# Optimization experiments

Hardware: AMD Instinct MI355X
Metric: run time of the kernel (lower is better)

The kernel has to match this reference:

```python
import jax, jax.numpy as jnp
import numpy as np
from jax import lax


def setup_inputs() -> dict:
    key = jax.random.key(0)
    ks = jax.random.split(key, 8)
    B, N, q = 16, 4096, 256
    sc = float(1.0 / np.sqrt(q))
    return {
        "u": jax.random.normal(ks[0], (B, N, q), jnp.float32),
        "a": jax.random.normal(ks[1], (q,), jnp.float32),  # diag of A
        "W_B": jax.random.normal(ks[2], (q, q), jnp.float32) * sc,
        "b_B": jax.random.normal(ks[3], (q,), jnp.float32) * sc,
        "W_C": jax.random.normal(ks[4], (q, q), jnp.float32) * sc,
        "b_C": jax.random.normal(ks[5], (q,), jnp.float32) * sc,
        "W_D": jax.random.normal(ks[6], (q, q), jnp.float32) * sc,
        "b_D": jax.random.normal(ks[7], (q,), jnp.float32) * sc,
    }


def _solve_im(u, a, W_B, b_B, dt):
    """IM solver. A is diagonal, so M_inv is four diagonal blocks:
    new_x = s*x - dt*s*a*z ; new_z = dt*s*x + s*z, with s = 1/(1+dt^2*a).
    Forcing F = M_inv @ [dt*B(u); 0] -> (dt*s*Bu, dt^2*s*Bu)."""
    s = 1.0 / (1.0 + dt * dt * a)  # (q,)
    Bu = jnp.einsum("bnq,pq->bnp", u, W_B) + b_B  # (B,N,q), torch Linear: u @ W^T + b
    f_x = (dt * s) * Bu
    f_z = (dt * dt * s) * Bu
    dsa = dt * s * a
    ds = dt * s

    def step(carry, f):
        x, z = carry
        fx, fz = f
        x_new = s * x - dsa * z + fx
        z_new = ds * x + s * z + fz
        return (x_new, z_new), z_new

    Bsz, _, q = u.shape
    init = (jnp.zeros((Bsz, q), u.dtype), jnp.zeros((Bsz, q), u.dtype))
    # scan over time axis
    _, z_t = lax.scan(step, init, (jnp.moveaxis(f_x, 1, 0), jnp.moveaxis(f_z, 1, 0)))
    return jnp.moveaxis(z_t, 0, 1)  # (B,N,q) -- the out[..., size:] half


def reference(u, a, W_B, b_B, W_C, b_C, W_D, b_D):
    N = u.shape[1]
    dt = 1.0 / N
    y = _solve_im(u, a, W_B, b_B, dt)
    x = (jnp.einsum("bnq,pq->bnp", y, W_C) + b_C) + (jnp.einsum("bnq,pq->bnp", u, W_D) + b_D)
    x = jax.nn.gelu(x, approximate=False)  # torch GELU default = exact erf
    # GLU(concat([x, x], -1)) == x * sigmoid(x)
    out = x * jax.nn.sigmoid(x) + u
    return (out, y)
```

## Files before the change

### kernel.cpp

```cpp
#include <hip/hip_runtime.h>
#include <hip/hip_bf16.h>
#include <cstdint>

typedef __bf16 bf16_t;
typedef __bf16 bf16x8 __attribute__((ext_vector_type(8)));
typedef float f32x4 __attribute__((ext_vector_type(4)));

#define B_SZ 16
#define N_SZ 4096
#define Q_SZ 256
#define M_TOT (B_SZ * N_SZ)
#define DT (1.0f / 4096.0f)
#define LDST 40
#define CHUNKS 64
#define LOG2_CLEN 6
#define CLEN (N_SZ / CHUNKS)
#define PF 8


__device__ __forceinline__ bf16x8 load8f(const float* p) {
  const float4 v0 = *(const float4*)p;
  const float4 v1 = *(const float4*)(p + 4);
  bf16x8 v;
  v[0] = (bf16_t)v0.x; v[1] = (bf16_t)v0.y; v[2] = (bf16_t)v0.z; v[3] = (bf16_t)v0.w;
  v[4] = (bf16_t)v1.x; v[5] = (bf16_t)v1.y; v[6] = (bf16_t)v1.z; v[7] = (bf16_t)v1.w;
  return v;
}

__device__ __forceinline__ int pidx(int tm, int tk, int lane) {
  return ((tm * 8 + tk) * 64 + lane) * 8;
}


__device__ __forceinline__ void kpassP(const bf16_t* __restrict__ A,
                                       const bf16_t* __restrict__ Bw,
                                       int tmA, int tnB, int lane,
                                       f32x4 acc[4][4]) {
#pragma unroll
  for (int tk = 0; tk < 8; ++tk) {
    bf16x8 af[4], bv[4];
#pragma unroll
    for (int i = 0; i < 4; ++i) {
      af[i] = *(const bf16x8*)(A + pidx(tmA + i, tk, lane));
      bv[i] = *(const bf16x8*)(Bw + pidx(tnB + i, tk, lane));
    }
#pragma unroll
    for (int mi = 0; mi < 4; ++mi)
#pragma unroll
      for (int ni = 0; ni < 4; ++ni)
        acc[mi][ni] = __builtin_amdgcn_mfma_f32_16x16x32_bf16(af[mi], bv[ni],
                                                              acc[mi][ni], 0, 0, 0);
  }
}

__device__ __forceinline__ void kpass2P(const bf16_t* __restrict__ A1,
                                        const bf16_t* __restrict__ B1,
                                        const bf16_t* __restrict__ A2,
                                        const bf16_t* __restrict__ B2,
                                        int tmA, int tnB, int lane,
                                        f32x4 acc[4][4]) {
#pragma unroll
  for (int tk = 0; tk < 8; ++tk) {
    bf16x8 a1[4], b1[4], a2[4], b2[4];
#pragma unroll
    for (int i = 0; i < 4; ++i) {
      a1[i] = *(const bf16x8*)(A1 + pidx(tmA + i, tk, lane));
      b1[i] = *(const bf16x8*)(B1 + pidx(tnB + i, tk, lane));
      a2[i] = *(const bf16x8*)(A2 + pidx(tmA + i, tk, lane));
      b2[i] = *(const bf16x8*)(B2 + pidx(tnB + i, tk, lane));
    }
#pragma unroll
    for (int mi = 0; mi < 4; ++mi)
#pragma unroll
      for (int ni = 0; ni < 4; ++ni)
        acc[mi][ni] = __builtin_amdgcn_mfma_f32_16x16x32_bf16(a1[mi], b1[ni],
                                                              acc[mi][ni], 0, 0, 0);
#pragma unroll
    for (int mi = 0; mi < 4; ++mi)
#pragma unroll
      for (int ni = 0; ni < 4; ++ni)
        acc[mi][ni] = __builtin_amdgcn_mfma_f32_16x16x32_bf16(a2[mi], b2[ni],
                                                              acc[mi][ni], 0, 0, 0);
  }
}

__global__ __launch_bounds__(256) void prep_kernel(
    const float* __restrict__ u, const float* __restrict__ WB,
    const float* __restrict__ WC, const float* __restrict__ WD,
    bf16_t* __restrict__ ubP, bf16_t* __restrict__ WBbP,
    bf16_t* __restrict__ WCbP, bf16_t* __restrict__ WDbP) {
  const int g = blockIdx.x * 256 + threadIdx.x;
  const int UC = (M_TOT * Q_SZ) / 8;
  const float* src;
  bf16_t* dst;
  int cidx;
  if (g < UC) {
    src = u; dst = ubP; cidx = g;
  } else {
    const int h = g - UC;
    const int w = h >> 13;
    cidx = h & 8191;
    src = (w == 0) ? WB : (w == 1) ? WC : WD;
    dst = (w == 0) ? WBbP : (w == 1) ? WCbP : WDbP;
  }
  const int lane = cidx & 63, tk = (cidx >> 6) & 7, tm = cidx >> 9;
  const int row = tm * 16 + (lane & 15);
  const int col = tk * 32 + (lane >> 4) * 8;
  *(bf16x8*)(dst + (size_t)cidx * 8) = load8f(src + (size_t)row * Q_SZ + col);
}

__global__ __launch_bounds__(256, 2) void gemm1p_kernel(
    const bf16_t* __restrict__ ubP, const bf16_t* __restrict__ WBbP,
    const float* __restrict__ a, const float* __restrict__ bB,
    float* __restrict__ fx) {
  const int t = threadIdx.x;
  const int bid = blockIdx.x;
  const int swz = (bid & 7) * 128 + (bid >> 3);
  const int m0 = (swz >> 1) * 128, n0 = (swz & 1) * 128;
  const int lane = t & 63, ln = lane & 15, quad = lane >> 4;
  const int wave = t >> 6;
  const int wm = (wave & 1) * 64, wn = (wave >> 1) * 64;
  f32x4 acc[4][4] = {};
  kpassP(ubP, WBbP, (m0 + wm) >> 4, (n0 + wn) >> 4, lane, acc);
#pragma unroll
  for (int ni = 0; ni < 4; ++ni) {
    const int gp = n0 + wn + ni * 16 + ln;
    const float av = a[gp];
    const float s = 1.0f / (1.0f + DT * DT * av);
    const float sc = DT * s;
    const float bb = bB[gp];
#pragma unroll
    for (int mi = 0; mi < 4; ++mi) {
      const int gm = m0 + wm + mi * 16 + quad * 4;
#pragma unroll
      for (int r2 = 0; r2 < 4; ++r2)
        fx[(size_t)(gm + r2) * Q_SZ + gp] = sc * (acc[mi][ni][r2] + bb);
    }
  }
}

__global__ __launch_bounds__(256, 2) void gemm2p_kernel(
    const bf16_t* __restrict__ ybP, const bf16_t* __restrict__ WCbP,
    const bf16_t* __restrict__ ubP, const bf16_t* __restrict__ WDbP,
    const float* __restrict__ u, const float* __restrict__ bC,
    const float* __restrict__ bD, float* __restrict__ out0) {
  const int t = threadIdx.x;
  const int bid = blockIdx.x;
  const int swz = (bid & 7) * 128 + (bid >> 3);
  const int m0 = (swz >> 1) * 128, n0 = (swz & 1) * 128;
  const int lane = t & 63, ln = lane & 15, quad = lane >> 4;
  const int wave = t >> 6;
  const int wm = (wave & 1) * 64, wn = (wave >> 1) * 64;
  f32x4 acc[4][4] = {};
  kpass2P(ybP, WCbP, ubP, WDbP, (m0 + wm) >> 4, (n0 + wn) >> 4, lane, acc);
#pragma unroll
  for (int ni = 0; ni < 4; ++ni) {
    const int gp = n0 + wn + ni * 16 + ln;
    const float bias = bC[gp] + bD[gp];
#pragma unroll
    for (int mi = 0; mi < 4; ++mi) {
      const int gm = m0 + wm + mi * 16 + quad * 4;
#pragma unroll
      for (int r2 = 0; r2 < 4; ++r2) {
        const float x = acc[mi][ni][r2] + bias;
        const float g = 0.5f * x * (1.0f + erff(x * 0.70710678118654752f));
        const float sg = 1.0f / (1.0f + __expf(-g));
        const float uu = u[(size_t)(gm + r2) * Q_SZ + gp];
        out0[(size_t)(gm + r2) * Q_SZ + gp] = fmaf(g, sg, uu);
      }
    }
  }
}


__global__ __launch_bounds__(256) void scan1_kernel(
    const float* __restrict__ fx, const float* __restrict__ a,
    float* __restrict__ ex, float* __restrict__ ez) {
  const int g = blockIdx.x * 256 + threadIdx.x;
  const int p = g & 255, c = (g >> 8) & (CHUNKS - 1), b = g >> 14;
  const float av = a[p];
  const float s = 1.0f / (1.0f + DT * DT * av);
  const float dsa = DT * s * av, dss = DT * s;
  float x = 0.f, z = 0.f;
  const float* fp = fx + ((size_t)b * N_SZ + c * CLEN) * Q_SZ + p;
  float buf[PF], nbuf[PF];
#pragma unroll
  for (int j = 0; j < PF; ++j) buf[j] = fp[(size_t)j * Q_SZ];
  for (int n = 0; n < CLEN; n += PF) {
    if (n + PF < CLEN) {
#pragma unroll
      for (int j = 0; j < PF; ++j) nbuf[j] = fp[(size_t)(n + PF + j) * Q_SZ];
    }
#pragma unroll
    for (int j = 0; j < PF; ++j) {
      const float f = buf[j];
      const float xn = fmaf(s, x, fmaf(-dsa, z, f));
      const float zn = fmaf(dss, x, fmaf(s, z, DT * f));
      x = xn; z = zn;
    }
#pragma unroll
    for (int j = 0; j < PF; ++j) buf[j] = nbuf[j];
  }
  ex[g] = x; ez[g] = z;
}

__global__ __launch_bounds__(256) void scan2_kernel(
    const float* __restrict__ a, const float* __restrict__ ex,
    const float* __restrict__ ez, float* __restrict__ ix, float* __restrict__ iz) {
  const int g = blockIdx.x * 256 + threadIdx.x;
  const int p = g & 255, b = g >> 8;
  const float av = a[p];
  const float s = 1.0f / (1.0f + DT * DT * av);
  float m00 = s, m01 = -DT * s * av, m10 = DT * s, m11 = s;
#pragma unroll
  for (int i = 0; i < LOG2_CLEN; ++i) {
    const float a00 = fmaf(m00, m00, m01 * m10);
    const float a01 = m01 * (m00 + m11);
    const float a10 = m10 * (m00 + m11);
    const float a11 = fmaf(m11, m11, m01 * m10);
    m00 = a00; m01 = a01; m10 = a10; m11 = a11;
  }
  float x = 0.f, z = 0.f;
  for (int c = 0; c < CHUNKS; ++c) {
    const size_t idx = ((size_t)b * CHUNKS + c) * Q_SZ + p;
    ix[idx] = x; iz[idx] = z;
    const float xn = fmaf(m00, x, fmaf(m01, z, ex[idx]));
    const float zn = fmaf(m10, x, fmaf(m11, z, ez[idx]));
    x = xn; z = zn;
  }
}

__global__ __launch_bounds__(256) void scan3_kernel(
    const float* __restrict__ a, const float* __restrict__ ix,
    const float* __restrict__ iz, float* __restrict__ yf,
    bf16_t* __restrict__ yb) {
  const int g = blockIdx.x * 256 + threadIdx.x;
  const int p = g & 255, c = (g >> 8) & (CHUNKS - 1), b = g >> 14;
  const float av = a[p];
  const float s = 1.0f / (1.0f + DT * DT * av);
  const float dsa = DT * s * av, dss = DT * s;
  float x = ix[g], z = iz[g];
  const size_t base = ((size_t)b * N_SZ + c * CLEN) * Q_SZ + p;
  float* yp = yf + base;
  const int tk = p >> 5, quad = (p >> 3) & 3, off = p & 7;
  const size_t ybase =
      ((size_t)(b * 256 + c * 4)) * 4096 + tk * 512 + quad * 128 + off;
  float buf[PF], nbuf[PF];
#pragma unroll
  for (int j = 0; j < PF; ++j) buf[j] = yp[(size_t)j * Q_SZ];
  for (int n = 0; n < CLEN; n += PF) {
    if (n + PF < CLEN) {
#pragma unroll
      for (int j = 0; j < PF; ++j) nbuf[j] = yp[(size_t)(n + PF + j) * Q_SZ];
    }
#pragma unroll
    for (int j = 0; j < PF; ++j) {
      const float f = buf[j];
      const float xn = fmaf(s, x, fmaf(-dsa, z, f));
      const float zn = fmaf(dss, x, fmaf(s, z, DT * f));
      x = xn; z = zn;
      yp[(size_t)(n + j) * Q_SZ] = zn;
      if (yb) {
        const int nj = n + j;
        yb[ybase + ((size_t)(nj >> 4) << 12) + ((nj & 15) << 3)] = (bf16_t)zn;
      }
    }
#pragma unroll
    for (int j = 0; j < PF; ++j) buf[j] = nbuf[j];
  }
}

__global__ __launch_bounds__(256) void scan_mono_kernel(
    const float* __restrict__ a, float* __restrict__ yf) {
  const int g = blockIdx.x * 256 + threadIdx.x;
  const int p = g & 255, b = g >> 8;
  const float av = a[p];
  const float s = 1.0f / (1.0f + DT * DT * av);
  const float dsa = DT * s * av, dss = DT * s;
  float x = 0.f, z = 0.f;
  float* yp = yf + (size_t)b * N_SZ * Q_SZ + p;
  float buf[PF], nbuf[PF];
#pragma unroll
  for (int j = 0; j < PF; ++j) buf[j] = yp[(size_t)j * Q_SZ];
  for (int n = 0; n < N_SZ; n += PF) {
    if (n + PF < N_SZ) {
#pragma unroll
      for (int j = 0; j < PF; ++j) nbuf[j] = yp[(size_t)(n + PF + j) * Q_SZ];
    }
#pragma unroll
    for (int j = 0; j < PF; ++j) {
      const float f = buf[j];
      const float xn = fmaf(s, x, fmaf(-dsa, z, f));
      const float zn = fmaf(dss, x, fmaf(s, z, DT * f));
      x = xn; z = zn;
      yp[(size_t)(n + j) * Q_SZ] = zn;
    }
#pragma unroll
    for (int j = 0; j < PF; ++j) buf[j] = nbuf[j];
  }
}


__device__ __forceinline__ void kloop(const float* __restrict__ Ap,
                                      const float* __restrict__ Bp,
                                      int m0, int n0, int t,
                                      bf16_t* As, bf16_t* Bs, f32x4 acc[4][4]) {
  const int r = t >> 2, cc = t & 3;
  const int lane = t & 63, ln = lane & 15, quad = lane >> 4;
  const int wave = t >> 6;
  const int wm = (wave & 1) * 64, wn = (wave >> 1) * 64;

  for (int k0 = 0; k0 < Q_SZ; k0 += 32) {
#pragma unroll
    for (int i = 0; i < 2; ++i) {
      const int row = r + i * 64;
      const int col = k0 + cc * 8;
      *(bf16x8*)(As + row * LDST + cc * 8) =
          load8f(Ap + (size_t)(m0 + row) * Q_SZ + col);
      *(bf16x8*)(Bs + row * LDST + cc * 8) =
          load8f(Bp + (size_t)(n0 + row) * Q_SZ + col);
    }
    __syncthreads();
    bf16x8 af[4], bv[4];
#pragma unroll
    for (int mi = 0; mi < 4; ++mi) {
      af[mi] = *(const bf16x8*)(As + (wm + mi * 16 + ln) * LDST + quad * 8);
      bv[mi] = *(const bf16x8*)(Bs + (wn + mi * 16 + ln) * LDST + quad * 8);
    }
#pragma unroll
    for (int mi = 0; mi < 4; ++mi)
#pragma unroll
      for (int ni = 0; ni < 4; ++ni)
        acc[mi][ni] = __builtin_amdgcn_mfma_f32_16x16x32_bf16(af[mi], bv[ni],
                                                              acc[mi][ni], 0, 0, 0);
    __syncthreads();
  }
}

__global__ __launch_bounds__(256) void gemm1_kernel(
    const float* __restrict__ u, const float* __restrict__ WB,
    const float* __restrict__ a, const float* __restrict__ bB,
    float* __restrict__ fx) {
  __shared__ __align__(16) bf16_t As[128 * LDST];
  __shared__ __align__(16) bf16_t Bs[128 * LDST];
  const int t = threadIdx.x;
  const int m0 = blockIdx.x * 128, n0 = blockIdx.y * 128;
  f32x4 acc[4][4] = {};
  kloop(u, WB, m0, n0, t, As, Bs, acc);

  const int lane = t & 63, ln = lane & 15, quad = lane >> 4;
  const int wave = t >> 6;
  const int wm = (wave & 1) * 64, wn = (wave >> 1) * 64;
#pragma unroll
  for (int ni = 0; ni < 4; ++ni) {
    const int gp = n0 + wn + ni * 16 + ln;
    const float av = a[gp];
    const float s = 1.0f / (1.0f + DT * DT * av);
    const float sc = DT * s;
    const float bb = bB[gp];
#pragma unroll
    for (int mi = 0; mi < 4; ++mi) {
      const int gm = m0 + wm + mi * 16 + quad * 4;
#pragma unroll
      for (int r2 = 0; r2 < 4; ++r2)
        fx[(size_t)(gm + r2) * Q_SZ + gp] = sc * (acc[mi][ni][r2] + bb);
    }
  }
}

__global__ __launch_bounds__(256) void gemm2_kernel(
    const float* __restrict__ y, const float* __restrict__ WC,
    const float* __restrict__ u, const float* __restrict__ WD,
    const float* __restrict__ bC, const float* __restrict__ bD,
    float* __restrict__ out0) {
  __shared__ __align__(16) bf16_t As[128 * LDST];
  __shared__ __align__(16) bf16_t Bs[128 * LDST];
  const int t = threadIdx.x;
  const int m0 = blockIdx.x * 128, n0 = blockIdx.y * 128;
  f32x4 acc[4][4] = {};
  kloop(y, WC, m0, n0, t, As, Bs, acc);
  kloop(u, WD, m0, n0, t, As, Bs, acc);

  const int lane = t & 63, ln = lane & 15, quad = lane >> 4;
  const int wave = t >> 6;
  const int wm = (wave & 1) * 64, wn = (wave >> 1) * 64;
#pragma unroll
  for (int ni = 0; ni < 4; ++ni) {
    const int gp = n0 + wn + ni * 16 + ln;
    const float bias = bC[gp] + bD[gp];
#pragma unroll
    for (int mi = 0; mi < 4; ++mi) {
      const int gm = m0 + wm + mi * 16 + quad * 4;
#pragma unroll
      for (int r2 = 0; r2 < 4; ++r2) {
        const float x = acc[mi][ni][r2] + bias;
        const float g = 0.5f * x * (1.0f + erff(x * 0.70710678118654752f));
        const float sg = 1.0f / (1.0f + __expf(-g));
        const float uu = u[(size_t)(gm + r2) * Q_SZ + gp];
        out0[(size_t)(gm + r2) * Q_SZ + gp] = fmaf(g, sg, uu);
      }
    }
  }
}


extern "C" void kernel_launch(void* const* d_in, const int* in_sizes, int n_in,
                              void* d_out, int out_size, void* d_ws, size_t ws_size,
                              hipStream_t stream) {
  const float* u  = (const float*)d_in[0];
  const float* a  = (const float*)d_in[1];
  const float* WB = (const float*)d_in[2];
  const float* bB = (const float*)d_in[3];
  const float* WC = (const float*)d_in[4];
  const float* bC = (const float*)d_in[5];
  const float* WD = (const float*)d_in[6];
  const float* bD = (const float*)d_in[7];

  float* out0 = (float*)d_out;
  float* yreg = out0 + (size_t)M_TOT * Q_SZ;

  const size_t UB_ELEMS = (size_t)M_TOT * Q_SZ;
  const size_t W_ELEMS = (size_t)Q_SZ * Q_SZ;
  const size_t state_bytes =
      4 * (size_t)B_SZ * CHUNKS * Q_SZ * sizeof(float);
  const size_t need_full =
      (2 * UB_ELEMS + 3 * W_ELEMS) * sizeof(bf16_t) + state_bytes;

  if (ws_size >= need_full) {
    bf16_t* ubP  = (bf16_t*)d_ws;
    bf16_t* ybP  = ubP + UB_ELEMS;
    bf16_t* WBbP = ybP + UB_ELEMS;
    bf16_t* WCbP = WBbP + W_ELEMS;
    bf16_t* WDbP = WCbP + W_ELEMS;
    float* ex = (float*)(WDbP + W_ELEMS);
    float* ez = ex + (size_t)B_SZ * CHUNKS * Q_SZ;
    float* ix = ez + (size_t)B_SZ * CHUNKS * Q_SZ;
    float* iz = ix + (size_t)B_SZ * CHUNKS * Q_SZ;

    prep_kernel<<<8288, 256, 0, stream>>>(u, WB, WC, WD, ubP, WBbP, WCbP, WDbP);
    gemm1p_kernel<<<1024, 256, 0, stream>>>(ubP, WBbP, a, bB, yreg);
    scan1_kernel<<<1024, 256, 0, stream>>>(yreg, a, ex, ez);
    scan2_kernel<<<16, 256, 0, stream>>>(a, ex, ez, ix, iz);
    scan3_kernel<<<1024, 256, 0, stream>>>(a, ix, iz, yreg, ybP);
    gemm2p_kernel<<<1024, 256, 0, stream>>>(ybP, WCbP, ubP, WDbP, u, bC, bD, out0);
  } else {
    dim3 gg(M_TOT / 128, Q_SZ / 128);
    gemm1_kernel<<<gg, 256, 0, stream>>>(u, WB, a, bB, yreg);
    if (ws_size >= state_bytes) {
      float* ex = (float*)d_ws;
      float* ez = ex + (size_t)B_SZ * CHUNKS * Q_SZ;
      float* ix = ez + (size_t)B_SZ * CHUNKS * Q_SZ;
      float* iz = ix + (size_t)B_SZ * CHUNKS * Q_SZ;
      scan1_kernel<<<1024, 256, 0, stream>>>(yreg, a, ex, ez);
      scan2_kernel<<<16, 256, 0, stream>>>(a, ex, ez, ix, iz);
      scan3_kernel<<<1024, 256, 0, stream>>>(a, ix, iz, yreg, (bf16_t*)nullptr);
    } else {
      scan_mono_kernel<<<16, 256, 0, stream>>>(a, yreg);
    }
    gemm2_kernel<<<gg, 256, 0, stream>>>(yreg, WC, u, WD, bC, bD, out0);
  }
}
```

Before: 331.0 us.

## Fuse chunk scan into GEMM epilogues using precomputed transition-matrix powers

The first GEMM now runs the local 64-step chunk scan in its epilogue through shared memory. It writes zero-initial local z values in a packed fp32 layout plus the chunk end states, so the separate scan1 kernel and the full fx round trip go away. A tiny kernel computes powers of the 2x2 transition matrix, and the second GEMM fixes up each local z with the carried-in chunk state (y = lz + T10*ix + T11*iz) while loading its A operand. It also converts to bf16 on the fly and writes y, removing scan3 and the bf16 y buffer. The cost is an fp32 lz buffer read inside the GEMM, extra loads for the correction terms, and a 64-step serial scan inside a GEMM block.

```diff
diff --git a/kernel.cpp b/kernel.cpp
--- a/kernel.cpp
+++ b/kernel.cpp
@@ -31,7 +31,6 @@
   return ((tm * 8 + tk) * 64 + lane) * 8;
 }
 
-
 __device__ __forceinline__ void kpassP(const bf16_t* __restrict__ A,
                                        const bf16_t* __restrict__ Bw,
                                        int tmA, int tnB, int lane,
@@ -49,37 +48,6 @@
 #pragma unroll
       for (int ni = 0; ni < 4; ++ni)
         acc[mi][ni] = __builtin_amdgcn_mfma_f32_16x16x32_bf16(af[mi], bv[ni],
-                                                              acc[mi][ni], 0, 0, 0);
-  }
-}
-
-__device__ __forceinline__ void kpass2P(const bf16_t* __restrict__ A1,
-                                        const bf16_t* __restrict__ B1,
-                                        const bf16_t* __restrict__ A2,
-                                        const bf16_t* __restrict__ B2,
-                                        int tmA, int tnB, int lane,
-                                        f32x4 acc[4][4]) {
-#pragma unroll
-  for (int tk = 0; tk < 8; ++tk) {
-    bf16x8 a1[4], b1[4], a2[4], b2[4];
-#pragma unroll
-    for (int i = 0; i < 4; ++i) {
-      a1[i] = *(const bf16x8*)(A1 + pidx(tmA + i, tk, lane));
-      b1[i] = *(const bf16x8*)(B1 + pidx(tnB + i, tk, lane));
-      a2[i] = *(const bf16x8*)(A2 + pidx(tmA + i, tk, lane));
-      b2[i] = *(const bf16x8*)(B2 + pidx(tnB + i, tk, lane));
-    }
-#pragma unroll
-    for (int mi = 0; mi < 4; ++mi)
-#pragma unroll
-      for (int ni = 0; ni < 4; ++ni)
-        acc[mi][ni] = __builtin_amdgcn_mfma_f32_16x16x32_bf16(a1[mi], b1[ni],
-                                                              acc[mi][ni], 0, 0, 0);
-#pragma unroll
-    for (int mi = 0; mi < 4; ++mi)
-#pragma unroll
-      for (int ni = 0; ni < 4; ++ni)
-        acc[mi][ni] = __builtin_amdgcn_mfma_f32_16x16x32_bf16(a2[mi], b2[ni],
                                                               acc[mi][ni], 0, 0, 0);
   }
 }
@@ -109,10 +77,12 @@
   *(bf16x8*)(dst + (size_t)cidx * 8) = load8f(src + (size_t)row * Q_SZ + col);
 }
 
-__global__ __launch_bounds__(256, 2) void gemm1p_kernel(
+__global__ __launch_bounds__(256, 2) void gemm1f_kernel(
     const bf16_t* __restrict__ ubP, const bf16_t* __restrict__ WBbP,
     const float* __restrict__ a, const float* __restrict__ bB,
-    float* __restrict__ fx) {
+    float* __restrict__ ex, float* __restrict__ ez,
+    float* __restrict__ lzP) {
+  __shared__ float T[2][64][128];
   const int t = threadIdx.x;
   const int bid = blockIdx.x;
   const int swz = (bid & 7) * 128 + (bid >> 3);
@@ -122,86 +92,50 @@
   const int wm = (wave & 1) * 64, wn = (wave >> 1) * 64;
   f32x4 acc[4][4] = {};
   kpassP(ubP, WBbP, (m0 + wm) >> 4, (n0 + wn) >> 4, lane, acc);
+
+  const int cc = wave & 1;
 #pragma unroll
   for (int ni = 0; ni < 4; ++ni) {
-    const int gp = n0 + wn + ni * 16 + ln;
+    const int colL = wn + ni * 16 + ln;
+    const int gp = n0 + colL;
     const float av = a[gp];
     const float s = 1.0f / (1.0f + DT * DT * av);
     const float sc = DT * s;
     const float bb = bB[gp];
 #pragma unroll
     for (int mi = 0; mi < 4; ++mi) {
-      const int gm = m0 + wm + mi * 16 + quad * 4;
+      const int nrow = mi * 16 + quad * 4;
 #pragma unroll
       for (int r2 = 0; r2 < 4; ++r2)
-        fx[(size_t)(gm + r2) * Q_SZ + gp] = sc * (acc[mi][ni][r2] + bb);
-    }
-  }
-}
-
-__global__ __launch_bounds__(256, 2) void gemm2p_kernel(
-    const bf16_t* __restrict__ ybP, const bf16_t* __restrict__ WCbP,
-    const bf16_t* __restrict__ ubP, const bf16_t* __restrict__ WDbP,
-    const float* __restrict__ u, const float* __restrict__ bC,
-    const float* __restrict__ bD, float* __restrict__ out0) {
-  const int t = threadIdx.x;
-  const int bid = blockIdx.x;
-  const int swz = (bid & 7) * 128 + (bid >> 3);
-  const int m0 = (swz >> 1) * 128, n0 = (swz & 1) * 128;
-  const int lane = t & 63, ln = lane & 15, quad = lane >> 4;
-  const int wave = t >> 6;
-  const int wm = (wave & 1) * 64, wn = (wave >> 1) * 64;
-  f32x4 acc[4][4] = {};
-  kpass2P(ybP, WCbP, ubP, WDbP, (m0 + wm) >> 4, (n0 + wn) >> 4, lane, acc);
-#pragma unroll
-  for (int ni = 0; ni < 4; ++ni) {
-    const int gp = n0 + wn + ni * 16 + ln;
-    const float bias = bC[gp] + bD[gp];
-#pragma unroll
-    for (int mi = 0; mi < 4; ++mi) {
-      const int gm = m0 + wm + mi * 16 + quad * 4;
-#pragma unroll
-      for (int r2 = 0; r2 < 4; ++r2) {
-        const float x = acc[mi][ni][r2] + bias;
-        const float g = 0.5f * x * (1.0f + erff(x * 0.70710678118654752f));
-        const float sg = 1.0f / (1.0f + __expf(-g));
-        const float uu = u[(size_t)(gm + r2) * Q_SZ + gp];
-        out0[(size_t)(gm + r2) * Q_SZ + gp] = fmaf(g, sg, uu);
-      }
-    }
-  }
-}
-
-
-__global__ __launch_bounds__(256) void scan1_kernel(
-    const float* __restrict__ fx, const float* __restrict__ a,
-    float* __restrict__ ex, float* __restrict__ ez) {
-  const int g = blockIdx.x * 256 + threadIdx.x;
-  const int p = g & 255, c = (g >> 8) & (CHUNKS - 1), b = g >> 14;
-  const float av = a[p];
-  const float s = 1.0f / (1.0f + DT * DT * av);
-  const float dsa = DT * s * av, dss = DT * s;
-  float x = 0.f, z = 0.f;
-  const float* fp = fx + ((size_t)b * N_SZ + c * CLEN) * Q_SZ + p;
-  float buf[PF], nbuf[PF];
-#pragma unroll
-  for (int j = 0; j < PF; ++j) buf[j] = fp[(size_t)j * Q_SZ];
-  for (int n = 0; n < CLEN; n += PF) {
-    if (n + PF < CLEN) {
-#pragma unroll
-      for (int j = 0; j < PF; ++j) nbuf[j] = fp[(size_t)(n + PF + j) * Q_SZ];
-    }
-#pragma unroll
-    for (int j = 0; j < PF; ++j) {
-      const float f = buf[j];
+        T[cc][nrow + r2][colL] = sc * (acc[mi][ni][r2] + bb);
+    }
+  }
+  __syncthreads();
+
+  const int scc = t >> 7, col = t & 127;
+  const int pg = n0 + col;
+  {
+    const float av = a[pg];
+    const float s = 1.0f / (1.0f + DT * DT * av);
+    const float dsa = DT * s * av, dss = DT * s;
+    const int mbase = m0 + scc * 64;
+    const int tkp = pg >> 5, e = pg & 7;
+    const int plane = (((pg >> 3) & 3) << 4);
+    float x = 0.f, z = 0.f;
+#pragma unroll 8
+    for (int n = 0; n < 64; ++n) {
+      const float f = T[scc][n][col];
       const float xn = fmaf(s, x, fmaf(-dsa, z, f));
       const float zn = fmaf(dss, x, fmaf(s, z, DT * f));
       x = xn; z = zn;
-    }
-#pragma unroll
-    for (int j = 0; j < PF; ++j) buf[j] = nbuf[j];
-  }
-  ex[g] = x; ez[g] = z;
+      const int m = mbase + n;
+      const int tm = m >> 4;
+      lzP[(size_t)(((tm * 8 + tkp) * 64 + (plane | (m & 15)))) * 8 + e] = zn;
+    }
+    const int chunk_g = mbase >> 6;
+    ex[chunk_g * 256 + pg] = x;
+    ez[chunk_g * 256 + pg] = z;
+  }
 }
 
 __global__ __launch_bounds__(256) void scan2_kernel(
@@ -230,73 +164,112 @@
   }
 }
 
-__global__ __launch_bounds__(256) void scan3_kernel(
-    const float* __restrict__ a, const float* __restrict__ ix,
-    const float* __restrict__ iz, float* __restrict__ yf,
-    bf16_t* __restrict__ yb) {
-  const int g = blockIdx.x * 256 + threadIdx.x;
-  const int p = g & 255, c = (g >> 8) & (CHUNKS - 1), b = g >> 14;
+__global__ __launch_bounds__(256) void mpow_kernel(
+    const float* __restrict__ a, float* __restrict__ t10,
+    float* __restrict__ t11) {
+  const int p = threadIdx.x;
   const float av = a[p];
   const float s = 1.0f / (1.0f + DT * DT * av);
-  const float dsa = DT * s * av, dss = DT * s;
-  float x = ix[g], z = iz[g];
-  const size_t base = ((size_t)b * N_SZ + c * CLEN) * Q_SZ + p;
-  float* yp = yf + base;
-  const int tk = p >> 5, quad = (p >> 3) & 3, off = p & 7;
-  const size_t ybase =
-      ((size_t)(b * 256 + c * 4)) * 4096 + tk * 512 + quad * 128 + off;
-  float buf[PF], nbuf[PF];
-#pragma unroll
-  for (int j = 0; j < PF; ++j) buf[j] = yp[(size_t)j * Q_SZ];
-  for (int n = 0; n < CLEN; n += PF) {
-    if (n + PF < CLEN) {
-#pragma unroll
-      for (int j = 0; j < PF; ++j) nbuf[j] = yp[(size_t)(n + PF + j) * Q_SZ];
-    }
-#pragma unroll
-    for (int j = 0; j < PF; ++j) {
-      const float f = buf[j];
-      const float xn = fmaf(s, x, fmaf(-dsa, z, f));
-      const float zn = fmaf(dss, x, fmaf(s, z, DT * f));
-      x = xn; z = zn;
-      yp[(size_t)(n + j) * Q_SZ] = zn;
-      if (yb) {
-        const int nj = n + j;
-        yb[ybase + ((size_t)(nj >> 4) << 12) + ((nj & 15) << 3)] = (bf16_t)zn;
+  const float m00 = s, m01 = -DT * s * av, m10 = DT * s, m11 = s;
+  float p00 = m00, p01 = m01, p10 = m10, p11 = m11;
+  for (int n = 0; n < 64; ++n) {
+    t10[n * 256 + p] = p10;
+    t11[n * 256 + p] = p11;
+    const float q00 = fmaf(m00, p00, m01 * p10);
+    const float q01 = fmaf(m00, p01, m01 * p11);
+    const float q10 = fmaf(m10, p00, m11 * p10);
+    const float q11 = fmaf(m10, p01, m11 * p11);
+    p00 = q00; p01 = q01; p10 = q10; p11 = q11;
+  }
+}
+
+__global__ __launch_bounds__(256, 2) void gemm2f_kernel(
+    const float* __restrict__ lzP, const bf16_t* __restrict__ WCbP,
+    const bf16_t* __restrict__ ubP, const bf16_t* __restrict__ WDbP,
+    const float* __restrict__ ix, const float* __restrict__ iz,
+    const float* __restrict__ t10, const float* __restrict__ t11,
+    const float* __restrict__ u, const float* __restrict__ bC,
+    const float* __restrict__ bD, float* __restrict__ yout,
+    float* __restrict__ out0) {
+  const int t = threadIdx.x;
+  const int bid = blockIdx.x;
+  const int swz = (bid & 7) * 128 + (bid >> 3);
+  const int m0 = (swz >> 1) * 128, n0 = (swz & 1) * 128;
+  const int lane = t & 63, ln = lane & 15, quad = lane >> 4;
+  const int wave = t >> 6;
+  const int wm = (wave & 1) * 64, wn = (wave >> 1) * 64;
+  const int tmA = (m0 + wm) >> 4, tnB = (n0 + wn) >> 4;
+  const bool wY = (n0 == 0) && (wn == 0);
+  f32x4 acc[4][4] = {};
+#pragma unroll
+  for (int tk = 0; tk < 8; ++tk) {
+    bf16x8 af[4], bv[4], a2[4], b2[4];
+#pragma unroll
+    for (int i = 0; i < 4; ++i) {
+      const float* lp = lzP + (size_t)(((tmA + i) * 8 + tk) * 64 + lane) * 8;
+      const f32x4 l0 = *(const f32x4*)lp;
+      const f32x4 l1 = *(const f32x4*)(lp + 4);
+      const int m = (tmA + i) * 16 + ln;
+      const int nloc = m & 63, cg = m >> 6;
+      const int p0 = tk * 32 + quad * 8;
+      const f32x4 tA0 = *(const f32x4*)(t10 + nloc * 256 + p0);
+      const f32x4 tA1 = *(const f32x4*)(t10 + nloc * 256 + p0 + 4);
+      const f32x4 tB0 = *(const f32x4*)(t11 + nloc * 256 + p0);
+      const f32x4 tB1 = *(const f32x4*)(t11 + nloc * 256 + p0 + 4);
+      const f32x4 X0 = *(const f32x4*)(ix + cg * 256 + p0);
+      const f32x4 X1 = *(const f32x4*)(ix + cg * 256 + p0 + 4);
+      const f32x4 Z0 = *(const f32x4*)(iz + cg * 256 + p0);
+      const f32x4 Z1 = *(const f32x4*)(iz + cg * 256 + p0 + 4);
+      f32x4 y0, y1;
+#pragma unroll
+      for (int e = 0; e < 4; ++e) {
+        y0[e] = fmaf(tA0[e], X0[e], fmaf(tB0[e], Z0[e], l0[e]));
+        y1[e] = fmaf(tA1[e], X1[e], fmaf(tB1[e], Z1[e], l1[e]));
       }
-    }
-#pragma unroll
-    for (int j = 0; j < PF; ++j) buf[j] = nbuf[j];
-  }
-}
-
-__global__ __launch_bounds__(256) void scan_mono_kernel(
-    const float* __restrict__ a, float* __restrict__ yf) {
-  const int g = blockIdx.x * 256 + threadIdx.x;
-  const int p = g & 255, b = g >> 8;
-  const float av = a[p];
-  const float s = 1.0f / (1.0f + DT * DT * av);
-  const float dsa = DT * s * av, dss = DT * s;
-  float x = 0.f, z = 0.f;
-  float* yp = yf + (size_t)b * N_SZ * Q_SZ + p;
-  float buf[PF], nbuf[PF];
-#pragma unroll
-  for (int j = 0; j < PF; ++j) buf[j] = yp[(size_t)j * Q_SZ];
-  for (int n = 0; n < N_SZ; n += PF) {
-    if (n + PF < N_SZ) {
-#pragma unroll
-      for (int j = 0; j < PF; ++j) nbuf[j] = yp[(size_t)(n + PF + j) * Q_SZ];
-    }
-#pragma unroll
-    for (int j = 0; j < PF; ++j) {
-      const float f = buf[j];
-      const float xn = fmaf(s, x, fmaf(-dsa, z, f));
-      const float zn = fmaf(dss, x, fmaf(s, z, DT * f));
-      x = xn; z = zn;
-      yp[(size_t)(n + j) * Q_SZ] = zn;
-    }
-#pragma unroll
-    for (int j = 0; j < PF; ++j) buf[j] = nbuf[j];
+      if (wY) {
+        *(f32x4*)(yout + (size_t)m * Q_SZ + p0) = y0;
+        *(f32x4*)(yout + (size_t)m * Q_SZ + p0 + 4) = y1;
+      }
+      bf16x8 av_;
+#pragma unroll
+      for (int e = 0; e < 4; ++e) {
+        av_[e] = (bf16_t)y0[e];
+        av_[e + 4] = (bf16_t)y1[e];
+      }
+      af[i] = av_;
+      a2[i] = *(const bf16x8*)(ubP + pidx(tmA + i, tk, lane));
+      bv[i] = *(const bf16x8*)(WCbP + pidx(tnB + i, tk, lane));
+      b2[i] = *(const bf16x8*)(WDbP + pidx(tnB + i, tk, lane));
+    }
+#pragma unroll
+    for (int mi = 0; mi < 4; ++mi)
+#pragma unroll
+      for (int ni = 0; ni < 4; ++ni)
+        acc[mi][ni] = __builtin_amdgcn_mfma_f32_16x16x32_bf16(af[mi], bv[ni],
+                                                              acc[mi][ni], 0, 0, 0);
+#pragma unroll
+    for (int mi = 0; mi < 4; ++mi)
+#pragma unroll
+      for (int ni = 0; ni < 4; ++ni)
+        acc[mi][ni] = __builtin_amdgcn_mfma_f32_16x16x32_bf16(a2[mi], b2[ni],
+                                                              acc[mi][ni], 0, 0, 0);
+  }
+#pragma unroll
+  for (int ni = 0; ni < 4; ++ni) {
+    const int gp = n0 + wn + ni * 16 + ln;
+    const float bias = bC[gp] + bD[gp];
+#pragma unroll
+    for (int mi = 0; mi < 4; ++mi) {
+      const int gm = m0 + wm + mi * 16 + quad * 4;
+#pragma unroll
+      for (int r2 = 0; r2 < 4; ++r2) {
+        const float x = acc[mi][ni][r2] + bias;
+        const float g = 0.5f * x * (1.0f + erff(x * 0.70710678118654752f));
+        const float sg = 1.0f / (1.0f + __expf(-g));
+        const float uu = u[(size_t)(gm + r2) * Q_SZ + gp];
+        out0[(size_t)(gm + r2) * Q_SZ + gp] = fmaf(g, sg, uu);
+      }
+    }
   }
 }
 
@@ -403,6 +376,62 @@
   }
 }
 
+__global__ __launch_bounds__(256) void scan1_kernel(
+    const float* __restrict__ fx, const float* __restrict__ a,
+    float* __restrict__ ex, float* __restrict__ ez) {
+  const int g = blockIdx.x * 256 + threadIdx.x;
+  const int p = g & 255, c = (g >> 8) & (CHUNKS - 1), b = g >> 14;
+  const float av = a[p];
+  const float s = 1.0f / (1.0f + DT * DT * av);
+  const float dsa = DT * s * av, dss = DT * s;
+  float x = 0.f, z = 0.f;
+  const float* fp = fx + ((size_t)b * N_SZ + c * CLEN) * Q_SZ + p;
+  for (int n = 0; n < CLEN; ++n) {
+    const float f = fp[(size_t)n * Q_SZ];
+    const float xn = fmaf(s, x, fmaf(-dsa, z, f));
+    const float zn = fmaf(dss, x, fmaf(s, z, DT * f));
+    x = xn; z = zn;
+  }
+  ex[g] = x; ez[g] = z;
+}
+
+__global__ __launch_bounds__(256) void scan3_kernel(
+    const float* __restrict__ a, const float* __restrict__ ix,
+    const float* __restrict__ iz, float* __restrict__ yf) {
+  const int g = blockIdx.x * 256 + threadIdx.x;
+  const int p = g & 255, c = (g >> 8) & (CHUNKS - 1), b = g >> 14;
+  const float av = a[p];
+  const float s = 1.0f / (1.0f + DT * DT * av);
+  const float dsa = DT * s * av, dss = DT * s;
+  float x = ix[g], z = iz[g];
+  float* yp = yf + ((size_t)b * N_SZ + c * CLEN) * Q_SZ + p;
+  for (int n = 0; n < CLEN; ++n) {
+    const float f = yp[(size_t)n * Q_SZ];
+    const float xn = fmaf(s, x, fmaf(-dsa, z, f));
+    const float zn = fmaf(dss, x, fmaf(s, z, DT * f));
+    x = xn; z = zn;
+    yp[(size_t)n * Q_SZ] = zn;
+  }
+}
+
+__global__ __launch_bounds__(256) void scan_mono_kernel(
+    const float* __restrict__ a, float* __restrict__ yf) {
+  const int g = blockIdx.x * 256 + threadIdx.x;
+  const int p = g & 255, b = g >> 8;
+  const float av = a[p];
+  const float s = 1.0f / (1.0f + DT * DT * av);
+  const float dsa = DT * s * av, dss = DT * s;
+  float x = 0.f, z = 0.f;
+  float* yp = yf + (size_t)b * N_SZ * Q_SZ + p;
+  for (int n = 0; n < N_SZ; ++n) {
+    const float f = yp[(size_t)n * Q_SZ];
+    const float xn = fmaf(s, x, fmaf(-dsa, z, f));
+    const float zn = fmaf(dss, x, fmaf(s, z, DT * f));
+    x = xn; z = zn;
+    yp[(size_t)n * Q_SZ] = zn;
+  }
+}
+
 
 extern "C" void kernel_launch(void* const* d_in, const int* in_sizes, int n_in,
                               void* d_out, int out_size, void* d_ws, size_t ws_size,
@@ -421,39 +450,43 @@
 
   const size_t UB_ELEMS = (size_t)M_TOT * Q_SZ;
   const size_t W_ELEMS = (size_t)Q_SZ * Q_SZ;
-  const size_t state_bytes =
-      4 * (size_t)B_SZ * CHUNKS * Q_SZ * sizeof(float);
+  const size_t ST_ELEMS = (size_t)B_SZ * CHUNKS * Q_SZ;
   const size_t need_full =
-      (2 * UB_ELEMS + 3 * W_ELEMS) * sizeof(bf16_t) + state_bytes;
+      UB_ELEMS * sizeof(bf16_t) + 3 * W_ELEMS * sizeof(bf16_t) +
+      UB_ELEMS * sizeof(float) + 4 * ST_ELEMS * sizeof(float) +
+      2 * 64 * 256 * sizeof(float);
+  const size_t state_bytes = 4 * ST_ELEMS * sizeof(float);
 
   if (ws_size >= need_full) {
     bf16_t* ubP  = (bf16_t*)d_ws;
-    bf16_t* ybP  = ubP + UB_ELEMS;
-    bf16_t* WBbP = ybP + UB_ELEMS;
+    bf16_t* WBbP = ubP + UB_ELEMS;
     bf16_t* WCbP = WBbP + W_ELEMS;
     bf16_t* WDbP = WCbP + W_ELEMS;
-    float* ex = (float*)(WDbP + W_ELEMS);
-    float* ez = ex + (size_t)B_SZ * CHUNKS * Q_SZ;
-    float* ix = ez + (size_t)B_SZ * CHUNKS * Q_SZ;
-    float* iz = ix + (size_t)B_SZ * CHUNKS * Q_SZ;
+    float* lzP = (float*)(WDbP + W_ELEMS);
+    float* ex = lzP + UB_ELEMS;
+    float* ez = ex + ST_ELEMS;
+    float* ix = ez + ST_ELEMS;
+    float* iz = ix + ST_ELEMS;
+    float* t10 = iz + ST_ELEMS;
+    float* t11 = t10 + 64 * 256;
 
     prep_kernel<<<8288, 256, 0, stream>>>(u, WB, WC, WD, ubP, WBbP, WCbP, WDbP);
-    gemm1p_kernel<<<1024, 256, 0, stream>>>(ubP, WBbP, a, bB, yreg);
-    scan1_kernel<<<1024, 256, 0, stream>>>(yreg, a, ex, ez);
+    gemm1f_kernel<<<1024, 256, 0, stream>>>(ubP, WBbP, a, bB, ex, ez, lzP);
     scan2_kernel<<<16, 256, 0, stream>>>(a, ex, ez, ix, iz);
-    scan3_kernel<<<1024, 256, 0, stream>>>(a, ix, iz, yreg, ybP);
-    gemm2p_kernel<<<1024, 256, 0, stream>>>(ybP, WCbP, ubP, WDbP, u, bC, bD, out0);
+    mpow_kernel<<<1, 256, 0, stream>>>(a, t10, t11);
+    gemm2f_kernel<<<1024, 256, 0, stream>>>(lzP, WCbP, ubP, WDbP, ix, iz,
+                                            t10, t11, u, bC, bD, yreg, out0);
   } else {
     dim3 gg(M_TOT / 128, Q_SZ / 128);
     gemm1_kernel<<<gg, 256, 0, stream>>>(u, WB, a, bB, yreg);
     if (ws_size >= state_bytes) {
       float* ex = (float*)d_ws;
-      float* ez = ex + (size_t)B_SZ * CHUNKS * Q_SZ;
-      float* ix = ez + (size_t)B_SZ * CHUNKS * Q_SZ;
-      float* iz = ix + (size_t)B_SZ * CHUNKS * Q_SZ;
+      float* ez = ex + ST_ELEMS;
+      float* ix = ez + ST_ELEMS;
+      float* iz = ix + ST_ELEMS;
       scan1_kernel<<<1024, 256, 0, stream>>>(yreg, a, ex, ez);
       scan2_kernel<<<16, 256, 0, stream>>>(a, ex, ez, ix, iz);
-      scan3_kernel<<<1024, 256, 0, stream>>>(a, ix, iz, yreg, (bf16_t*)nullptr);
+      scan3_kernel<<<1024, 256, 0, stream>>>(a, ix, iz, yreg);
     } else {
       scan_mono_kernel<<<16, 256, 0, stream>>>(a, yreg);
     }
```

Result: slower. 395.0 us (+19.3%).
